# Kernel optimization log

Measured on AMD Instinct MI355X. Metric: run time of the kernel, lower is better.

The kernel has to match this reference:

```python
import jax, jax.numpy as jnp
import numpy as np

B, N, D, H = 2, 2048, 1024, 16
HD = D // H

def setup_inputs() -> dict:
    key = jax.random.key(0)
    ks = jax.random.split(key, 5)
    s_in = 1.0 / np.sqrt(D)
    x = jax.random.normal(ks[0], (B, N, D), dtype=jnp.float32)
    W_qkv = jax.random.uniform(ks[1], (3 * D, D), minval=-s_in, maxval=s_in, dtype=jnp.float32)
    b_qkv = jax.random.uniform(ks[2], (3 * D,), minval=-s_in, maxval=s_in, dtype=jnp.float32)
    W_out = jax.random.uniform(ks[3], (D, D), minval=-s_in, maxval=s_in, dtype=jnp.float32)
    b_out = jax.random.uniform(ks[4], (D,), minval=-s_in, maxval=s_in, dtype=jnp.float32)
    return {"x": x, "W_qkv": W_qkv, "b_qkv": b_qkv, "W_out": W_out, "b_out": b_out}

def reference(x, W_qkv, b_qkv, W_out, b_out):
    scale = HD ** (-0.5)
    qkv = x @ W_qkv.T + b_qkv                       # [B,N,3D]
    q, k, v = jnp.split(qkv, 3, axis=-1)
    # [B,N,D] -> [B,H,N,HD]
    def heads(t):
        return t.reshape(B, N, H, HD).transpose(0, 2, 1, 3)
    q, k, v = heads(q), heads(k), heads(v)
    attn = jnp.einsum('bhqd,bhkd->bhqk', q, k) * scale   # [B,H,N,N]
    causal = jnp.tril(jnp.ones((N, N), dtype=bool))
    attn = jnp.where(causal, attn, -jnp.inf)
    attn = jax.nn.softmax(attn, axis=-1)
    out = jnp.einsum('bhqk,bhkd->bhqd', attn, v)         # [B,H,N,HD]
    out = out.transpose(0, 2, 1, 3).reshape(B, N, D)
    return out @ W_out.T + b_out
```

## Files before the change

### kernel.cpp

```cpp
#include <hip/hip_runtime.h>
#include <hip/hip_bf16.h>

#define Bdim 2
#define Nseq 2048
#define Dmod 1024
#define Hn   16
#define HDim 64

#define XN  (Bdim * Nseq * Dmod)
#define WQN (3 * Dmod * Dmod)
#define WON (Dmod * Dmod)

typedef __attribute__((ext_vector_type(8))) __bf16 bf16x8;
typedef __attribute__((ext_vector_type(4))) __bf16 bf16x4;
typedef __attribute__((ext_vector_type(4))) float  floatx4;

__device__ __forceinline__ floatx4 mfma16(bf16x8 a, bf16x8 b, floatx4 c) {
    return __builtin_amdgcn_mfma_f32_16x16x32_bf16(a, b, c, 0, 0, 0);
}

__device__ __forceinline__ float exp2v(float x) {
    return __builtin_amdgcn_exp2f(x);
}

__device__ __forceinline__ void async_copy16(__bf16* l, const __bf16* g) {
    __builtin_amdgcn_global_load_lds(
        (const __attribute__((address_space(1))) void*)g,
        (__attribute__((address_space(3))) void*)l,
        16, 0, 0);
}

__global__ __launch_bounds__(256) void convert_kernel(
    const float* __restrict__ x, const float* __restrict__ wq,
    const float* __restrict__ wo,
    __bf16* __restrict__ xb, __bf16* __restrict__ wqb, __bf16* __restrict__ wob)
{
    int i = (blockIdx.x * 256 + threadIdx.x) * 8;
    const float* src;
    __bf16* dst;
    int off;
    if (i < XN)            { src = x;  dst = xb;  off = i; }
    else if (i < XN + WQN) { src = wq; dst = wqb; off = i - XN; }
    else                   { src = wo; dst = wob; off = i - XN - WQN; }
    float4 v0 = *(const float4*)(src + off);
    float4 v1 = *(const float4*)(src + off + 4);
    bf16x8 o;
    o[0] = (__bf16)v0.x; o[1] = (__bf16)v0.y; o[2] = (__bf16)v0.z; o[3] = (__bf16)v0.w;
    o[4] = (__bf16)v1.x; o[5] = (__bf16)v1.y; o[6] = (__bf16)v1.z; o[7] = (__bf16)v1.w;
    *(bf16x8*)(dst + off) = o;
}

__global__ __launch_bounds__(256) void qkv_kernel(
    const __bf16* __restrict__ x, const __bf16* __restrict__ Wq,
    const float* __restrict__ bq,
    __bf16* __restrict__ qb, __bf16* __restrict__ kb, __bf16* __restrict__ vt)
{
    __shared__ __align__(16) __bf16 ldsA[128 * 32];
    __shared__ __align__(16) __bf16 ldsB[128 * 32];

    const int tid  = threadIdx.x;
    const int lane = tid & 63, l16 = lane & 15, quad = lane >> 4;
    const int wiw  = tid >> 6;
    const int wm   = wiw & 1, wn = wiw >> 1;

    const int bm = blockIdx.x & 31;
    const int bn = blockIdx.x >> 5;
    const int m0 = bm * 128, n0 = bn * 128;

    const int srow = tid >> 2;
    const int scol = (tid & 3) * 8;

    floatx4 z = {0.f, 0.f, 0.f, 0.f};
    floatx4 acc[4][4];
    #pragma unroll
    for (int mt = 0; mt < 4; ++mt)
        #pragma unroll
        for (int nt = 0; nt < 4; ++nt) acc[mt][nt] = z;

    const __bf16* ga = x  + (size_t)m0 * Dmod;
    const __bf16* gb = Wq + (size_t)n0 * Dmod;

    for (int k0 = 0; k0 < Dmod; k0 += 32) {
        async_copy16(&ldsA[srow * 32 + scol],        ga + (size_t)srow * Dmod + k0 + scol);
        async_copy16(&ldsA[(64 + srow) * 32 + scol], ga + (size_t)(64 + srow) * Dmod + k0 + scol);
        async_copy16(&ldsB[srow * 32 + scol],        gb + (size_t)srow * Dmod + k0 + scol);
        async_copy16(&ldsB[(64 + srow) * 32 + scol], gb + (size_t)(64 + srow) * Dmod + k0 + scol);
        __syncthreads();

        bf16x8 af[4], bfr[4];
        #pragma unroll
        for (int mt = 0; mt < 4; ++mt)
            af[mt] = *(const bf16x8*)&ldsA[(wm * 64 + mt * 16 + l16) * 32 + quad * 8];
        #pragma unroll
        for (int nt = 0; nt < 4; ++nt)
            bfr[nt] = *(const bf16x8*)&ldsB[(wn * 64 + nt * 16 + l16) * 32 + quad * 8];
        #pragma unroll
        for (int mt = 0; mt < 4; ++mt)
            #pragma unroll
            for (int nt = 0; nt < 4; ++nt)
                acc[mt][nt] = mfma16(af[mt], bfr[nt], acc[mt][nt]);
        __syncthreads();
    }

    const int nb    = n0 + wn * 64;
    const int which = nb >> 10;
    const int h     = (nb & 1023) >> 6;
    const int mw    = m0 + wm * 64;
    const int bi    = mw >> 11;
    const int pos0  = mw & (Nseq - 1);

    #pragma unroll
    for (int nt = 0; nt < 4; ++nt) {
        float bias = bq[nb + nt * 16 + l16];
        int hd = nt * 16 + l16;
        #pragma unroll
        for (int mt = 0; mt < 4; ++mt)
            #pragma unroll
            for (int i = 0; i < 4; ++i) {
                int pos = pos0 + mt * 16 + quad * 4 + i;
                __bf16 v = (__bf16)(acc[mt][nt][i] + bias);
                if (which == 0)
                    qb[((bi * Hn + h) * Nseq + pos) * HDim + hd] = v;
                else if (which == 1)
                    kb[((bi * Hn + h) * Nseq + pos) * HDim + hd] = v;
                else
                    vt[((bi * Hn + h) * HDim + hd) * Nseq + pos] = v;
            }
    }
}

__global__ __launch_bounds__(256, 4) void attn_kernel(
    const __bf16* __restrict__ qbuf, const __bf16* __restrict__ kbuf,
    const __bf16* __restrict__ vtbuf, __bf16* __restrict__ aout)
{
    __shared__ __align__(16) __bf16 ldsK[64 * 64];
    __shared__ __align__(16) __bf16 ldsV[64 * 64];
    __shared__ __align__(16) __bf16 ldsP[4][16 * 72];

    const int tid  = threadIdx.x;
    const int wiw  = tid >> 6;
    const int lane = tid & 63, l16 = lane & 15, quad = lane >> 4;
    const int b    = blockIdx.x;
    const int bh   = b & 31;
    const int qblk = 31 - (b >> 5);
    const int q0   = qblk * 64 + wiw * 16;

    const __bf16* qs = qbuf  + bh * Nseq * HDim;
    const __bf16* ks = kbuf  + bh * Nseq * HDim;
    const __bf16* vs = vtbuf + bh * HDim * Nseq;

    const int sr  = tid >> 3;
    const int sb  = tid & 7;
    const int swr = (sb ^ (sr & 7)) * 8;
    const int wk0 = sr * 64 + swr;
    const int wk1 = (sr + 32) * 64 + swr;

    bf16x8 qf0 = *(const bf16x8*)(qs + (q0 + l16) * HDim + quad * 8);
    bf16x8 qf1 = *(const bf16x8*)(qs + (q0 + l16) * HDim + 32 + quad * 8);

    floatx4 z = {0.f, 0.f, 0.f, 0.f};
    floatx4 o[4];
    #pragma unroll
    for (int s = 0; s < 4; ++s) o[s] = z;
    float m_i = -1e30f, l_i = 0.f;

    const float C   = 0.125f * 1.44269504f;
    const int   nkt = qblk + 1;
    __bf16* myp = ldsP[wiw];
    const int swz = l16 & 7;

    float4 rk0 = *(const float4*)(ks + (size_t)sr * HDim + sb * 8);
    float4 rk1 = *(const float4*)(ks + (size_t)(sr + 32) * HDim + sb * 8);
    float4 rv0 = *(const float4*)(vs + (size_t)sr * Nseq + sb * 8);
    float4 rv1 = *(const float4*)(vs + (size_t)(sr + 32) * Nseq + sb * 8);

    for (int kt = 0; kt < nkt; ++kt) {
        float4 nk0 = {}, nk1 = {}, nv0 = {}, nv1 = {};
        if (kt + 1 < nkt) {
            const int k0n = (kt + 1) * 64;
            nk0 = *(const float4*)(ks + (size_t)(k0n + sr) * HDim + sb * 8);
            nk1 = *(const float4*)(ks + (size_t)(k0n + sr + 32) * HDim + sb * 8);
            nv0 = *(const float4*)(vs + (size_t)sr * Nseq + k0n + sb * 8);
            nv1 = *(const float4*)(vs + (size_t)(sr + 32) * Nseq + k0n + sb * 8);
        }

        *(float4*)&ldsK[wk0] = rk0;
        *(float4*)&ldsK[wk1] = rk1;
        *(float4*)&ldsV[wk0] = rv0;
        *(float4*)&ldsV[wk1] = rv1;
        __syncthreads();

        const bool last = (kt == nkt - 1);

        floatx4 st[4];
        #pragma unroll
        for (int t = 0; t < 4; ++t) {
            const __bf16* kr = &ldsK[(t * 16 + l16) * 64];
            bf16x8 kf0 = *(const bf16x8*)(kr + ((quad ^ swz) * 8));
            bf16x8 kf1 = *(const bf16x8*)(kr + (((quad + 4) ^ swz) * 8));
            st[t] = mfma16(kf0, qf0, z);
            st[t] = mfma16(kf1, qf1, st[t]);
        }

        float a[16];
        #pragma unroll
        for (int t = 0; t < 4; ++t)
            #pragma unroll
            for (int i = 0; i < 4; ++i) {
                float v = st[t][i] * C;
                if (last) {
                    int kidx = t * 16 + quad * 4 + i;
                    v = (kidx <= wiw * 16 + l16) ? v : -1e30f;
                }
                a[t * 4 + i] = v;
            }

        float mA = fmaxf(fmaxf(a[0], a[1]),  fmaxf(a[2], a[3]));
        float mB = fmaxf(fmaxf(a[4], a[5]),  fmaxf(a[6], a[7]));
        float mC = fmaxf(fmaxf(a[8], a[9]),  fmaxf(a[10], a[11]));
        float mD = fmaxf(fmaxf(a[12], a[13]), fmaxf(a[14], a[15]));
        float mx = fmaxf(fmaxf(mA, mB), fmaxf(mC, mD));
        mx = fmaxf(mx, __shfl_xor(mx, 16));
        mx = fmaxf(mx, __shfl_xor(mx, 32));

        float mn    = fmaxf(m_i, mx);
        float alpha = exp2v(m_i - mn);

        float p[16];
        #pragma unroll
        for (int j = 0; j < 16; ++j) p[j] = exp2v(a[j] - mn);
        float sA = (p[0] + p[1]) + (p[2] + p[3]);
        float sB = (p[4] + p[5]) + (p[6] + p[7]);
        float sC = (p[8] + p[9]) + (p[10] + p[11]);
        float sD = (p[12] + p[13]) + (p[14] + p[15]);
        float rs = (sA + sB) + (sC + sD);
        rs += __shfl_xor(rs, 16);
        rs += __shfl_xor(rs, 32);
        l_i = l_i * alpha + rs;
        m_i = mn;

        #pragma unroll
        for (int s = 0; s < 4; ++s)
            #pragma unroll
            for (int i = 0; i < 4; ++i) o[s][i] *= alpha;

        #pragma unroll
        for (int t = 0; t < 4; ++t) {
            bf16x4 pk;
            pk.x = (__bf16)p[t * 4 + 0]; pk.y = (__bf16)p[t * 4 + 1];
            pk.z = (__bf16)p[t * 4 + 2]; pk.w = (__bf16)p[t * 4 + 3];
            *(bf16x4*)(myp + l16 * 72 + t * 16 + quad * 4) = pk;
        }
        asm volatile("s_waitcnt lgkmcnt(0)" ::: "memory");
        bf16x8 pf0 = *(const bf16x8*)(myp + l16 * 72 + quad * 8);
        bf16x8 pf1 = *(const bf16x8*)(myp + l16 * 72 + 32 + quad * 8);

        #pragma unroll
        for (int s = 0; s < 4; ++s) {
            const __bf16* vr = &ldsV[(s * 16 + l16) * 64];
            bf16x8 vf0 = *(const bf16x8*)(vr + ((quad ^ swz) * 8));
            bf16x8 vf1 = *(const bf16x8*)(vr + (((quad + 4) ^ swz) * 8));
            o[s] = mfma16(vf0, pf0, o[s]);
            o[s] = mfma16(vf1, pf1, o[s]);
        }
        __syncthreads();

        rk0 = nk0; rk1 = nk1; rv0 = nv0; rv1 = nv1;
    }

    const float inv = 1.0f / l_i;
    const int bi = bh >> 4, h = bh & 15;
    #pragma unroll
    for (int s = 0; s < 4; ++s) {
        bf16x4 ov;
        ov.x = (__bf16)(o[s][0] * inv); ov.y = (__bf16)(o[s][1] * inv);
        ov.z = (__bf16)(o[s][2] * inv); ov.w = (__bf16)(o[s][3] * inv);
        *(bf16x4*)(aout + ((size_t)(bi * Nseq + q0 + l16)) * Dmod
                   + h * 64 + s * 16 + quad * 4) = ov;
    }
}

__global__ __launch_bounds__(256) void proj_kernel(
    const __bf16* __restrict__ ao, const __bf16* __restrict__ Wo,
    const float* __restrict__ bo, float* __restrict__ out)
{
    __shared__ __align__(16) __bf16 ldsA[64 * 32];
    __shared__ __align__(16) __bf16 ldsB[128 * 32];

    const int tid  = threadIdx.x;
    const int lane = tid & 63, l16 = lane & 15, quad = lane >> 4;
    const int wiw  = tid >> 6;
    const int wm   = wiw & 1, wn = wiw >> 1;

    const int bm = blockIdx.x & 63;
    const int bn = blockIdx.x >> 6;
    const int m0 = bm * 64, n0 = bn * 128;

    const int srow = tid >> 2;
    const int scol = (tid & 3) * 8;

    floatx4 z = {0.f, 0.f, 0.f, 0.f};
    floatx4 acc[2][4];
    #pragma unroll
    for (int mt = 0; mt < 2; ++mt)
        #pragma unroll
        for (int nt = 0; nt < 4; ++nt) acc[mt][nt] = z;

    const __bf16* ga = ao + (size_t)m0 * Dmod;
    const __bf16* gb = Wo + (size_t)n0 * Dmod;

    for (int k0 = 0; k0 < Dmod; k0 += 32) {
        async_copy16(&ldsA[srow * 32 + scol],        ga + (size_t)srow * Dmod + k0 + scol);
        async_copy16(&ldsB[srow * 32 + scol],        gb + (size_t)srow * Dmod + k0 + scol);
        async_copy16(&ldsB[(64 + srow) * 32 + scol], gb + (size_t)(64 + srow) * Dmod + k0 + scol);
        __syncthreads();

        bf16x8 af[2], bfr[4];
        #pragma unroll
        for (int mt = 0; mt < 2; ++mt)
            af[mt] = *(const bf16x8*)&ldsA[(wm * 32 + mt * 16 + l16) * 32 + quad * 8];
        #pragma unroll
        for (int nt = 0; nt < 4; ++nt)
            bfr[nt] = *(const bf16x8*)&ldsB[(wn * 64 + nt * 16 + l16) * 32 + quad * 8];
        #pragma unroll
        for (int mt = 0; mt < 2; ++mt)
            #pragma unroll
            for (int nt = 0; nt < 4; ++nt)
                acc[mt][nt] = mfma16(af[mt], bfr[nt], acc[mt][nt]);
        __syncthreads();
    }

    const int nb = n0 + wn * 64;
    const int mw = m0 + wm * 32;
    #pragma unroll
    for (int nt = 0; nt < 4; ++nt) {
        float bias = bo[nb + nt * 16 + l16];
        #pragma unroll
        for (int mt = 0; mt < 2; ++mt)
            #pragma unroll
            for (int i = 0; i < 4; ++i) {
                int m = mw + mt * 16 + quad * 4 + i;
                out[(size_t)m * Dmod + nb + nt * 16 + l16] = acc[mt][nt][i] + bias;
            }
    }
}

extern "C" void kernel_launch(void* const* d_in, const int* in_sizes, int n_in,
                              void* d_out, int out_size, void* d_ws, size_t ws_size,
                              hipStream_t stream) {
    const float* x  = (const float*)d_in[0];
    const float* Wq = (const float*)d_in[1];
    const float* bq = (const float*)d_in[2];
    const float* Wo = (const float*)d_in[3];
    const float* bo = (const float*)d_in[4];
    float* out = (float*)d_out;

    __bf16* ws  = (__bf16*)d_ws;
    __bf16* xb  = ws;
    __bf16* wqb = ws + (size_t)XN;
    __bf16* wob = wqb + (size_t)WQN;
    __bf16* qb  = wob + (size_t)WON;
    const size_t SZ = (size_t)Bdim * Hn * Nseq * HDim;
    __bf16* kb  = qb + SZ;
    __bf16* vt  = kb + SZ;
    __bf16* ao  = vt + SZ;

    convert_kernel<<<dim3(4096), dim3(256), 0, stream>>>(x, Wq, Wo, xb, wqb, wob);
    qkv_kernel<<<dim3(768), dim3(256), 0, stream>>>(xb, wqb, bq, qb, kb, vt);
    attn_kernel<<<dim3(1024), dim3(256), 0, stream>>>(qb, kb, vt, ao);
    proj_kernel<<<dim3(512), dim3(256), 0, stream>>>(ao, wob, bo, out);
}
```

Measured before the change: 185.6 us.

## Fold softmax scale into Q, lazy rescaling, MFMA row sums, balanced causal scheduling

Folds the softmax scale and log2e factor into Q when the QKV projection writes it out, which removes a multiply per score. The online-softmax max is only updated when the new max exceeds the running max by more than 8, so the rescale of O and l is skipped most of the time. Row sums now come from an extra MFMA against a ones vector instead of adds and shuffles. It also interleaves causal q-block order across the launch to balance load, and raises wave priority around the MFMA sections. The lazy rescale relies on bounded growth of exp2, and summing bf16-rounded P values changes numerics slightly.

```diff
diff --git a/kernel.cpp b/kernel.cpp
--- a/kernel.cpp
+++ b/kernel.cpp
@@ -109,6 +109,8 @@
     const int bi    = mw >> 11;
     const int pos0  = mw & (Nseq - 1);
 
+    const float qscale = 0.18033688f;
+
     #pragma unroll
     for (int nt = 0; nt < 4; ++nt) {
         float bias = bq[nb + nt * 16 + l16];
@@ -118,13 +120,13 @@
             #pragma unroll
             for (int i = 0; i < 4; ++i) {
                 int pos = pos0 + mt * 16 + quad * 4 + i;
-                __bf16 v = (__bf16)(acc[mt][nt][i] + bias);
+                float r = acc[mt][nt][i] + bias;
                 if (which == 0)
-                    qb[((bi * Hn + h) * Nseq + pos) * HDim + hd] = v;
+                    qb[((bi * Hn + h) * Nseq + pos) * HDim + hd] = (__bf16)(r * qscale);
                 else if (which == 1)
-                    kb[((bi * Hn + h) * Nseq + pos) * HDim + hd] = v;
+                    kb[((bi * Hn + h) * Nseq + pos) * HDim + hd] = (__bf16)r;
                 else
-                    vt[((bi * Hn + h) * HDim + hd) * Nseq + pos] = v;
+                    vt[((bi * Hn + h) * HDim + hd) * Nseq + pos] = (__bf16)r;
             }
     }
 }
@@ -142,8 +144,15 @@
     const int lane = tid & 63, l16 = lane & 15, quad = lane >> 4;
     const int b    = blockIdx.x;
     const int bh   = b & 31;
-    const int qblk = 31 - (b >> 5);
-    const int q0   = qblk * 64 + wiw * 16;
+    const int g  = b >> 5;
+    const int gk = g & 7, r4 = g >> 3;
+    int qblk;
+    if      (r4 == 0) qblk = 31 - gk;
+    else if (r4 == 1) qblk = gk;
+    else if (r4 == 2) qblk = 23 - gk;
+    else              qblk = 8 + gk;
+
+    const int q0 = qblk * 64 + wiw * 16;
 
     const __bf16* qs = qbuf  + bh * Nseq * HDim;
     const __bf16* ks = kbuf  + bh * Nseq * HDim;
@@ -162,9 +171,13 @@
     floatx4 o[4];
     #pragma unroll
     for (int s = 0; s < 4; ++s) o[s] = z;
-    float m_i = -1e30f, l_i = 0.f;
-
-    const float C   = 0.125f * 1.44269504f;
+    floatx4 lacc = z;
+    float m_i = -1e30f;
+
+    bf16x8 ones;
+    #pragma unroll
+    for (int j = 0; j < 8; ++j) ones[j] = (__bf16)1.0f;
+
     const int   nkt = qblk + 1;
     __bf16* myp = ldsP[wiw];
     const int swz = l16 & 7;
@@ -193,6 +206,7 @@
         const bool last = (kt == nkt - 1);
 
         floatx4 st[4];
+        __builtin_amdgcn_s_setprio(1);
         #pragma unroll
         for (int t = 0; t < 4; ++t) {
             const __bf16* kr = &ldsK[(t * 16 + l16) * 64];
@@ -201,13 +215,14 @@
             st[t] = mfma16(kf0, qf0, z);
             st[t] = mfma16(kf1, qf1, st[t]);
         }
+        __builtin_amdgcn_s_setprio(0);
 
         float a[16];
         #pragma unroll
         for (int t = 0; t < 4; ++t)
             #pragma unroll
             for (int i = 0; i < 4; ++i) {
-                float v = st[t][i] * C;
+                float v = st[t][i];
                 if (last) {
                     int kidx = t * 16 + quad * 4 + i;
                     v = (kidx <= wiw * 16 + l16) ? v : -1e30f;
@@ -215,34 +230,31 @@
                 a[t * 4 + i] = v;
             }
 
-        float mA = fmaxf(fmaxf(a[0], a[1]),  fmaxf(a[2], a[3]));
-        float mB = fmaxf(fmaxf(a[4], a[5]),  fmaxf(a[6], a[7]));
-        float mC = fmaxf(fmaxf(a[8], a[9]),  fmaxf(a[10], a[11]));
-        float mD = fmaxf(fmaxf(a[12], a[13]), fmaxf(a[14], a[15]));
-        float mx = fmaxf(fmaxf(mA, mB), fmaxf(mC, mD));
+        float m0 = fmaxf(fmaxf(a[0],  a[1]),  a[2]);
+        float m1 = fmaxf(fmaxf(a[3],  a[4]),  a[5]);
+        float m2 = fmaxf(fmaxf(a[6],  a[7]),  a[8]);
+        float m3 = fmaxf(fmaxf(a[9],  a[10]), a[11]);
+        float m4 = fmaxf(fmaxf(a[12], a[13]), a[14]);
+        float mx = fmaxf(fmaxf(fmaxf(m0, m1), m2),
+                         fmaxf(fmaxf(m3, m4), a[15]));
         mx = fmaxf(mx, __shfl_xor(mx, 16));
         mx = fmaxf(mx, __shfl_xor(mx, 32));
 
-        float mn    = fmaxf(m_i, mx);
-        float alpha = exp2v(m_i - mn);
+        if (__any(mx > m_i + 8.0f)) {
+            float mn    = fmaxf(m_i, mx);
+            float alpha = exp2v(m_i - mn);
+            #pragma unroll
+            for (int s = 0; s < 4; ++s)
+                #pragma unroll
+                for (int i = 0; i < 4; ++i) o[s][i] *= alpha;
+            #pragma unroll
+            for (int i = 0; i < 4; ++i) lacc[i] *= alpha;
+            m_i = mn;
+        }
 
         float p[16];
         #pragma unroll
-        for (int j = 0; j < 16; ++j) p[j] = exp2v(a[j] - mn);
-        float sA = (p[0] + p[1]) + (p[2] + p[3]);
-        float sB = (p[4] + p[5]) + (p[6] + p[7]);
-        float sC = (p[8] + p[9]) + (p[10] + p[11]);
-        float sD = (p[12] + p[13]) + (p[14] + p[15]);
-        float rs = (sA + sB) + (sC + sD);
-        rs += __shfl_xor(rs, 16);
-        rs += __shfl_xor(rs, 32);
-        l_i = l_i * alpha + rs;
-        m_i = mn;
-
-        #pragma unroll
-        for (int s = 0; s < 4; ++s)
-            #pragma unroll
-            for (int i = 0; i < 4; ++i) o[s][i] *= alpha;
+        for (int j = 0; j < 16; ++j) p[j] = exp2v(a[j] - m_i);
 
         #pragma unroll
         for (int t = 0; t < 4; ++t) {
@@ -254,6 +266,10 @@
         asm volatile("s_waitcnt lgkmcnt(0)" ::: "memory");
         bf16x8 pf0 = *(const bf16x8*)(myp + l16 * 72 + quad * 8);
         bf16x8 pf1 = *(const bf16x8*)(myp + l16 * 72 + 32 + quad * 8);
+
+        __builtin_amdgcn_s_setprio(1);
+        lacc = mfma16(ones, pf0, lacc);
+        lacc = mfma16(ones, pf1, lacc);
 
         #pragma unroll
         for (int s = 0; s < 4; ++s) {
@@ -263,12 +279,13 @@
             o[s] = mfma16(vf0, pf0, o[s]);
             o[s] = mfma16(vf1, pf1, o[s]);
         }
+        __builtin_amdgcn_s_setprio(0);
         __syncthreads();
 
         rk0 = nk0; rk1 = nk1; rv0 = nv0; rv1 = nv1;
     }
 
-    const float inv = 1.0f / l_i;
+    const float inv = 1.0f / lacc[0];
     const int bi = bh >> 4, h = bh & 15;
     #pragma unroll
     for (int s = 0; s < 4; ++s) {
```

Result: faster. 174.5 us (-5.9%).
